# Kernel optimization log

Hardware: AMD Instinct MI355X
Metric: run time of the kernel (lower is better)

Reference implementation:

```python
import jax, jax.numpy as jnp
import numpy as np

EMBED = 256
HEADS = 8
LEVELS = 4
POINTS = 4
HD = EMBED // HEADS  # 32
SHAPES = [(100, 100), (50, 50), (25, 25), (13, 13)]  # (H, W) per level
NV = sum(h * w for h, w in SHAPES)  # 13294
BS = 2


def _lin_params(k, fan_in, fan_out):
    s = 1.0 / np.sqrt(fan_in)
    kw, kb = jax.random.split(k)
    W = jax.random.uniform(kw, (fan_in, fan_out), jnp.float32, -s, s)
    b = jax.random.uniform(kb, (fan_out,), jnp.float32, -s, s)
    return W, b


def setup_inputs():
    key = jax.random.key(0)
    ks = jax.random.split(key, 10)
    inp = {
        "query": jax.random.normal(ks[0], (BS, NV, EMBED), jnp.float32),
        "key": jax.random.normal(ks[1], (BS, NV, EMBED), jnp.float32),
        "value": jax.random.normal(ks[2], (BS, NV, EMBED), jnp.float32),
        "query_pos": jax.random.normal(ks[3], (BS, NV, EMBED), jnp.float32),
        "reference_points": jax.random.uniform(ks[4], (BS, NV, LEVELS, 2), jnp.float32),
        "spatial_shapes": jnp.array(SHAPES, jnp.int32),
        "level_start_index": jnp.array(np.cumsum([0] + [h * w for h, w in SHAPES[:-1]]), jnp.int32),
        "key_padding_mask": jnp.zeros((BS, NV), bool),
    }
    inp["W_value"], inp["b_value"] = _lin_params(ks[5], EMBED, EMBED)
    inp["W_off"], inp["b_off"] = _lin_params(ks[6], EMBED, HEADS * LEVELS * POINTS * 2)
    inp["W_attn"], inp["b_attn"] = _lin_params(ks[7], EMBED, HEADS * LEVELS * POINTS)
    inp["W_out"], inp["b_out"] = _lin_params(ks[8], EMBED, EMBED)
    inp["W_ffn"], inp["b_ffn"] = _lin_params(ks[9], EMBED, EMBED)
    return inp


def _bilinear(v, x, y, H, W):
    # v: (bs, heads, H*W, hd); x, y: (bs, heads, n) pixel coords (align_corners=False)
    # zero padding outside the feature map (matches torch grid_sample padding_mode='zeros')
    x0 = jnp.floor(x)
    y0 = jnp.floor(y)
    lx = x - x0
    ly = y - y0
    x0 = x0.astype(jnp.int32)
    y0 = y0.astype(jnp.int32)

    def g(xi, yi):
        valid = ((xi >= 0) & (xi < W) & (yi >= 0) & (yi < H)).astype(v.dtype)
        idx = jnp.clip(yi, 0, H - 1) * W + jnp.clip(xi, 0, W - 1)
        return jnp.take_along_axis(v, idx[..., None], axis=2) * valid[..., None]

    return (g(x0, y0) * ((1 - lx) * (1 - ly))[..., None]
            + g(x0 + 1, y0) * (lx * (1 - ly))[..., None]
            + g(x0, y0 + 1) * ((1 - lx) * ly)[..., None]
            + g(x0 + 1, y0 + 1) * (lx * ly)[..., None])


def _forward(query, key, value, query_pos, reference_points, shapes, starts,
             key_padding_mask, W_value, b_value, W_off, b_off, W_attn, b_attn,
             W_out, b_out, W_ffn, b_ffn):
    bs, nq, _ = query.shape
    identity = query  # residual taken BEFORE adding positional encoding (mmcv semantics)
    q = query + query_pos
    v = value @ W_value + b_value
    v = jnp.where(key_padding_mask[..., None], 0.0, v).reshape(bs, -1, HEADS, HD)
    off = (q @ W_off + b_off).reshape(bs, nq, HEADS, LEVELS, POINTS, 2)
    aw = jax.nn.softmax((q @ W_attn + b_attn).reshape(bs, nq, HEADS, LEVELS * POINTS), axis=-1)
    aw = aw.reshape(bs, nq, HEADS, LEVELS, POINTS)
    # offset normalizer is (W, H) per level
    wh = jnp.array([[w, h] for h, w in shapes], jnp.float32)
    loc = reference_points[:, :, None, :, None, :] + off / wh[None, None, None, :, None, :]
    out = jnp.zeros((bs, HEADS, nq, HD), q.dtype)
    for l, (H, W) in enumerate(shapes):
        s = starts[l]
        vl = v[:, s:s + H * W].transpose(0, 2, 1, 3)  # (bs, heads, H*W, hd)
        x = (loc[:, :, :, l, :, 0] * W - 0.5).transpose(0, 2, 1, 3).reshape(bs, HEADS, nq * POINTS)
        y = (loc[:, :, :, l, :, 1] * H - 0.5).transpose(0, 2, 1, 3).reshape(bs, HEADS, nq * POINTS)
        smp = _bilinear(vl, x, y, H, W).reshape(bs, HEADS, nq, POINTS, HD)
        wl = aw[:, :, :, l].transpose(0, 2, 1, 3)  # (bs, heads, nq, P)
        out = out + jnp.sum(smp * wl[..., None], axis=3)
    out = out.transpose(0, 2, 1, 3).reshape(bs, nq, EMBED)
    out = out @ W_out + b_out + identity
    return out @ W_ffn + b_ffn


def reference(query, key, value, query_pos, reference_points, spatial_shapes,
              level_start_index, key_padding_mask, W_value, b_value, W_off, b_off,
              W_attn, b_attn, W_out, b_out, W_ffn, b_ffn):
    # spatial shapes / level starts are structural metadata -> treat as static ints
    shapes = [tuple(int(x) for x in r) for r in np.asarray(spatial_shapes)]
    starts = [int(x) for x in np.asarray(level_start_index)]
    return _forward(query, key, value, query_pos, reference_points, shapes, starts,
                    key_padding_mask, W_value, b_value, W_off, b_off, W_attn, b_attn,
                    W_out, b_out, W_ffn, b_ffn)
```

## Files before the change

### kernel.cpp

```cpp
#include <hip/hip_runtime.h>
#include <hip/hip_bf16.h>
#include <math.h>

#define NQ 13294
#define NV 13294
#define M_ROWS (2*NQ)
#define MP 26624

typedef __attribute__((ext_vector_type(8))) short bf16x8;
typedef __attribute__((ext_vector_type(4))) float f32x4;
typedef __attribute__((ext_vector_type(2))) float f32x2;

__device__ __forceinline__ float4 ld4(const float* p){ return *(const float4*)p; }
__device__ __forceinline__ float bfu_lo(unsigned int u){ return __uint_as_float(u << 16); }
__device__ __forceinline__ float bfu_hi(unsigned int u){ return __uint_as_float(u & 0xffff0000u); }
__device__ __forceinline__ unsigned short f2bf(float f){
  unsigned int u = __float_as_uint(f);
  u += 0x7fffu + ((u >> 16) & 1u);
  return (unsigned short)(u >> 16);
}
__device__ __forceinline__ unsigned int pk2(float a, float b){
  return (unsigned int)f2bf(a) | ((unsigned int)f2bf(b) << 16);
}
__device__ __forceinline__ void gl_lds16(const unsigned short* g, unsigned short* l) {
  __builtin_amdgcn_global_load_lds(
      (const __attribute__((address_space(1))) unsigned int*)g,
      (__attribute__((address_space(3))) unsigned int*)l, 16, 0, 0);
}

__global__ __launch_bounds__(256) void prep_all(
    const float* __restrict__ value, const float* __restrict__ query,
    const float* __restrict__ qpos,
    unsigned short* __restrict__ val_bf, unsigned short* __restrict__ q_bf,
    const float* __restrict__ wv, const float* __restrict__ wo,
    const float* __restrict__ wa, const float* __restrict__ wu,
    const float* __restrict__ wf, unsigned short* __restrict__ wt)
{
  const int total = MP * 64;
  for (int i = blockIdx.x * 256 + threadIdx.x; i < total; i += gridDim.x * 256) {
    const int e = i * 4;
    ushort4 a = make_ushort4(0,0,0,0), b = make_ushort4(0,0,0,0);
    if (e < M_ROWS * 256) {
      float4 v4 = ld4(value + e);
      a = make_ushort4(f2bf(v4.x), f2bf(v4.y), f2bf(v4.z), f2bf(v4.w));
      float4 q4 = ld4(query + e);
      float4 p4 = ld4(qpos + e);
      b = make_ushort4(f2bf(q4.x+p4.x), f2bf(q4.y+p4.y), f2bf(q4.z+p4.z), f2bf(q4.w+p4.w));
    }
    *(ushort4*)(val_bf + e) = a;
    *(ushort4*)(q_bf   + e) = b;
  }
  for (int t = blockIdx.x * 256 + threadIdx.x; t < 294912; t += gridDim.x * 256) {
    const float* src; int Nn; int base;
    if      (t < 65536)  { src = wv; Nn = 256; base = 0; }
    else if (t < 131072) { src = wo; Nn = 256; base = 65536; }
    else if (t < 163840) { src = wa; Nn = 128; base = 131072; }
    else if (t < 229376) { src = wu; Nn = 256; base = 163840; }
    else                 { src = wf; Nn = 256; base = 229376; }
    const int local = t - base;
    const int n = local >> 8, k = local & 255;
    wt[t] = f2bf(src[k * Nn + n]);
  }
}

template<int NCOL, int OUT_MODE, bool ADD_RES>
__global__ __launch_bounds__(256) void gemm_gl(
    const unsigned short* __restrict__ A, const unsigned short* __restrict__ Bt,
    const float* __restrict__ biasA, const float* __restrict__ biasB,
    const float* __restrict__ RES, void* __restrict__ Cv, int N)
{
  __shared__ unsigned short lds[32768];

  const int nwg = 416 * NCOL;
  const int lin = blockIdx.x;
  const int swz = (lin & 7) * (nwg >> 3) + (lin >> 3);
  const int brow = (swz / NCOL) * 64;
  const int bcol = (swz % NCOL) * 64;

  const int tid  = threadIdx.x;
  const int wid  = tid >> 6, lane = tid & 63;
  const int wr   = wid >> 1, wc = wid & 1;
  const int fr   = lane & 15, fg = lane >> 4;

  {
    const int r0   = lane >> 3;
    const int slot = lane & 7;
    #pragma unroll
    for (int t = 0; t < 4; ++t) {
      #pragma unroll
      for (int c = 0; c < 2; ++c) {
        const int row = (wid * 2 + c) * 8 + r0;
        const int gsl = slot ^ (row & 7);
        gl_lds16(A  + (size_t)(brow + row) * 256 + t * 64 + (gsl << 3),
                 &lds[t * 4096 + (wid * 2 + c) * 512]);
        gl_lds16(Bt + (size_t)(bcol + row) * 256 + t * 64 + (gsl << 3),
                 &lds[16384 + t * 4096 + (wid * 2 + c) * 512]);
      }
    }
  }
  __syncthreads();

  f32x4 acc[2][2];
  #pragma unroll
  for (int m = 0; m < 2; ++m)
    #pragma unroll
    for (int n = 0; n < 2; ++n)
      acc[m][n] = (f32x4){0.f, 0.f, 0.f, 0.f};

  #pragma unroll
  for (int t = 0; t < 4; ++t) {
    const char* as = (const char*)&lds[t * 4096];
    const char* bs = (const char*)&lds[16384 + t * 4096];
    #pragma unroll
    for (int kk = 0; kk < 2; ++kk) {
      const int kb = kk * 64 + fg * 16;
      bf16x8 af[2], bfv[2];
      #pragma unroll
      for (int m = 0; m < 2; ++m) {
        const int r = wr * 32 + m * 16 + fr;
        af[m] = *(const bf16x8*)(as + r * 128 + (kb ^ ((r & 7) << 4)));
      }
      #pragma unroll
      for (int n = 0; n < 2; ++n) {
        const int r = wc * 32 + n * 16 + fr;
        bfv[n] = *(const bf16x8*)(bs + r * 128 + (kb ^ ((r & 7) << 4)));
      }
      #pragma unroll
      for (int m = 0; m < 2; ++m)
        #pragma unroll
        for (int n = 0; n < 2; ++n)
          acc[m][n] = __builtin_amdgcn_mfma_f32_16x16x32_bf16(af[m], bfv[n], acc[m][n], 0, 0, 0);
    }
  }

  __syncthreads();
  float* csh = (float*)lds;
  const int c0 = bcol + wc * 32 + fr;
  const int c1 = c0 + 16;
  const float bn0 = (c0 < 256) ? biasA[c0] : biasB[c0 - 256];
  const float bn1 = (c1 < 256) ? biasA[c1] : biasB[c1 - 256];
  #pragma unroll
  for (int m = 0; m < 2; ++m)
    #pragma unroll
    for (int j = 0; j < 4; ++j) {
      const int row = wr * 32 + m * 16 + fg * 4 + j;
      csh[row * 64 + wc * 32 + fr]      = acc[m][0][j] + bn0;
      csh[row * 64 + wc * 32 + 16 + fr] = acc[m][1][j] + bn1;
    }
  __syncthreads();
  #pragma unroll
  for (int i = 0; i < 4; ++i) {
    const int rl = i * 16 + (tid >> 4);
    const int gr = brow + rl;
    if (gr >= M_ROWS) continue;
    const int c4 = (tid & 15) * 4;
    float4 v = *(const float4*)&csh[rl * 64 + c4];
    if (ADD_RES) {
      float4 q = ld4(RES + (size_t)gr * 256 + bcol + c4);
      v.x += q.x; v.y += q.y; v.z += q.z; v.w += q.w;
    }
    if (OUT_MODE == 0) {
      *(float4*)&((float*)Cv)[(size_t)gr * N + bcol + c4] = v;
    } else if (OUT_MODE == 1) {
      ushort4 pk = make_ushort4(f2bf(v.x), f2bf(v.y), f2bf(v.z), f2bf(v.w));
      *(ushort4*)&((unsigned short*)Cv)[(size_t)gr * N + bcol + c4] = pk;
    } else {
      const int head = (bcol + c4) >> 5;
      const int ch   = c4 & 31;
      int r = 0;
      r = __builtin_amdgcn_cvt_pk_fp8_f32(v.x, v.y, r, 0);
      r = __builtin_amdgcn_cvt_pk_fp8_f32(v.z, v.w, r, 1);
      *(int*)&((unsigned char*)Cv)[((size_t)head * M_ROWS + gr) * 32 + ch] = r;
    }
  }
}

__global__ __launch_bounds__(256) void msda7(
    const unsigned char* __restrict__ v, const unsigned short* __restrict__ oa,
    const float* __restrict__ ref, unsigned short* __restrict__ attout)
{
  constexpr int LW[4] = {100, 50, 25, 13};
  constexpr int LS[4] = {0, 10000, 12500, 13125};

  __shared__ int2   sidx[64][17];
  __shared__ float4 swt [64][17];

  const int bid   = blockIdx.x;
  const int h     = bid & 7;
  const int chunk = bid >> 3;
  const int tid   = threadIdx.x;
  const int q     = tid >> 2;
  const int c     = tid & 3;
  const int bq    = chunk * 64 + q;
  const bool active = bq < M_ROWS;
  const int b     = (bq >= NQ) ? 1 : 0;

  if (active) {
    const int l = c;
    const int W = LW[l];
    const float fD = (float)W;
    const unsigned short* oarow = oa + (size_t)bq * 384;

    uint2 lg = *(const uint2*)(oarow + 256 + h * 16 + l * 4);
    float g0 = bfu_lo(lg.x), g1 = bfu_hi(lg.x), g2 = bfu_lo(lg.y), g3 = bfu_hi(lg.y);
    float mx = fmaxf(fmaxf(g0, g1), fmaxf(g2, g3));
    mx = fmaxf(mx, __shfl_xor(mx, 1));
    mx = fmaxf(mx, __shfl_xor(mx, 2));
    float e0 = __expf(g0-mx), e1 = __expf(g1-mx), e2 = __expf(g2-mx), e3 = __expf(g3-mx);
    float s = e0 + e1 + e2 + e3;
    s += __shfl_xor(s, 1);
    s += __shfl_xor(s, 2);
    const float inv = 1.f / s;
    const float ee[4] = {e0*inv, e1*inv, e2*inv, e3*inv};

    uint4 ov = *(const uint4*)(oarow + h * 32 + l * 8);
    const float oxy[8] = {bfu_lo(ov.x), bfu_hi(ov.x), bfu_lo(ov.y), bfu_hi(ov.y),
                          bfu_lo(ov.z), bfu_hi(ov.z), bfu_lo(ov.w), bfu_hi(ov.w)};
    const float rx = ref[(size_t)bq * 8 + l * 2];
    const float ry = ref[(size_t)bq * 8 + l * 2 + 1];
    const int rowbase = b * NV + LS[l];

    #pragma unroll
    for (int j = 0; j < 4; ++j) {
      const float x = fmaf(rx, fD, oxy[2*j])   - 0.5f;
      const float y = fmaf(ry, fD, oxy[2*j+1]) - 0.5f;
      const float x0f = floorf(x), y0f = floorf(y);
      const float lx = x - x0f, ly = y - y0f;
      const int x0 = (int)x0f, y0 = (int)y0f;
      const int y1 = y0 + 1;
      const int xbase = min(max(x0, 0), W - 2);
      const float wx0 = 1.f - lx, wx1 = lx;
      const float we0 = (x0 == xbase     ? wx0 : 0.f) + (x0 == xbase - 1 ? wx1 : 0.f);
      const float we1 = (x0 == xbase + 1 ? wx0 : 0.f) + (x0 == xbase     ? wx1 : 0.f);
      const int cy0 = min(max(y0, 0), W - 1), cy1 = min(max(y1, 0), W - 1);
      const float wy0 = (y0 >= 0 && y0 < W) ? (1.f - ly) : 0.f;
      const float wy1 = (y1 >= 0 && y1 < W) ? ly : 0.f;
      const float wt = ee[j];
      const int p = l * 4 + j;
      sidx[q][p] = make_int2((rowbase + cy0 * W + xbase) * 32,
                             (rowbase + cy1 * W + xbase) * 32);
      swt[q][p] = make_float4(wt * wy0 * we0, wt * wy0 * we1,
                              wt * wy1 * we0, wt * wy1 * we1);
    }
  }
  __syncthreads();

  if (active) {
    const unsigned char* vb = v + (size_t)h * M_ROWS * 32 + c * 16;
    const int el = c >> 1;
    f32x2 acc2[8];
    #pragma unroll
    for (int k = 0; k < 8; ++k) acc2[k] = (f32x2){0.f, 0.f};
    #pragma unroll
    for (int p = 0; p < 16; ++p) {
      const int2   ix = sidx[q][p];
      const float4 w4 = swt[q][p];
      uint4 r0 = *(const uint4*)(vb + ix.x);
      uint4 r1 = *(const uint4*)(vb + ix.y);
      const float wa = el ? w4.y : w4.x;
      const float wb = el ? w4.w : w4.z;
      const f32x2 wav = (f32x2){wa, wa};
      const f32x2 wbv = (f32x2){wb, wb};
      acc2[0] = wav * __builtin_amdgcn_cvt_pk_f32_fp8(r0.x, 0) + acc2[0];
      acc2[1] = wav * __builtin_amdgcn_cvt_pk_f32_fp8(r0.x, 1) + acc2[1];
      acc2[2] = wav * __builtin_amdgcn_cvt_pk_f32_fp8(r0.y, 0) + acc2[2];
      acc2[3] = wav * __builtin_amdgcn_cvt_pk_f32_fp8(r0.y, 1) + acc2[3];
      acc2[4] = wav * __builtin_amdgcn_cvt_pk_f32_fp8(r0.z, 0) + acc2[4];
      acc2[5] = wav * __builtin_amdgcn_cvt_pk_f32_fp8(r0.z, 1) + acc2[5];
      acc2[6] = wav * __builtin_amdgcn_cvt_pk_f32_fp8(r0.w, 0) + acc2[6];
      acc2[7] = wav * __builtin_amdgcn_cvt_pk_f32_fp8(r0.w, 1) + acc2[7];
      acc2[0] = wbv * __builtin_amdgcn_cvt_pk_f32_fp8(r1.x, 0) + acc2[0];
      acc2[1] = wbv * __builtin_amdgcn_cvt_pk_f32_fp8(r1.x, 1) + acc2[1];
      acc2[2] = wbv * __builtin_amdgcn_cvt_pk_f32_fp8(r1.y, 0) + acc2[2];
      acc2[3] = wbv * __builtin_amdgcn_cvt_pk_f32_fp8(r1.y, 1) + acc2[3];
      acc2[4] = wbv * __builtin_amdgcn_cvt_pk_f32_fp8(r1.z, 0) + acc2[4];
      acc2[5] = wbv * __builtin_amdgcn_cvt_pk_f32_fp8(r1.z, 1) + acc2[5];
      acc2[6] = wbv * __builtin_amdgcn_cvt_pk_f32_fp8(r1.w, 0) + acc2[6];
      acc2[7] = wbv * __builtin_amdgcn_cvt_pk_f32_fp8(r1.w, 1) + acc2[7];
    }
    #pragma unroll
    for (int k = 0; k < 8; ++k) {
      acc2[k][0] += __shfl_xor(acc2[k][0], 2);
      acc2[k][1] += __shfl_xor(acc2[k][1], 2);
    }
    if (c < 2) {
      uint4 pkA, pkB;
      pkA.x = pk2(acc2[0][0], acc2[0][1]);
      pkA.y = pk2(acc2[1][0], acc2[1][1]);
      pkA.z = pk2(acc2[2][0], acc2[2][1]);
      pkA.w = pk2(acc2[3][0], acc2[3][1]);
      pkB.x = pk2(acc2[4][0], acc2[4][1]);
      pkB.y = pk2(acc2[5][0], acc2[5][1]);
      pkB.z = pk2(acc2[6][0], acc2[6][1]);
      pkB.w = pk2(acc2[7][0], acc2[7][1]);
      unsigned short* dst = attout + (size_t)bq * 256 + h * 32 + c * 16;
      *(uint4*)dst = pkA;
      *(uint4*)(dst + 8) = pkB;
    }
  }
}

extern "C" void kernel_launch(void* const* d_in, const int* in_sizes, int n_in,
                              void* d_out, int out_size, void* d_ws, size_t ws_size,
                              hipStream_t stream) {
  const float* query  = (const float*)d_in[0];
  const float* value  = (const float*)d_in[2];
  const float* qpos   = (const float*)d_in[3];
  const float* refpts = (const float*)d_in[4];
  const float* W_value = (const float*)d_in[8];
  const float* b_value = (const float*)d_in[9];
  const float* W_off   = (const float*)d_in[10];
  const float* b_off   = (const float*)d_in[11];
  const float* W_attn  = (const float*)d_in[12];
  const float* b_attn  = (const float*)d_in[13];
  const float* W_out   = (const float*)d_in[14];
  const float* b_out   = (const float*)d_in[15];
  const float* W_ffn   = (const float*)d_in[16];
  const float* b_ffn   = (const float*)d_in[17];
  float* out = (float*)d_out;

  unsigned short* oa    = (unsigned short*)d_ws;
  unsigned char*  vbuf8 = (unsigned char*)(oa + (size_t)MP * 384);
  unsigned short* AB1   = (unsigned short*)(vbuf8 + (size_t)8 * M_ROWS * 32);
  unsigned short* AB2   = AB1 + (size_t)MP * 256;
  unsigned short* wts   = AB2 + (size_t)MP * 256;
  unsigned short* wv_t  = wts;
  unsigned short* woa_t = wts + 65536;
  unsigned short* wu_t  = wts + 163840;
  unsigned short* wf_t  = wts + 229376;

  const dim3 blk(256);

  prep_all<<<dim3(2048), blk, 0, stream>>>(value, query, qpos, AB1, AB2,
      W_value, W_off, W_attn, W_out, W_ffn, wts);

  gemm_gl<4,2,false><<<dim3(1664), blk, 0, stream>>>(
      AB1, wv_t, b_value, b_value, nullptr, vbuf8, 256);
  gemm_gl<6,1,false><<<dim3(2496), blk, 0, stream>>>(
      AB2, woa_t, b_off, b_attn, nullptr, oa, 384);
  msda7<<<dim3(8 * 416), blk, 0, stream>>>(vbuf8, oa, refpts, AB1);
  gemm_gl<4,1,true><<<dim3(1664), blk, 0, stream>>>(
      AB1, wu_t, b_out, b_out, query, AB2, 256);
  gemm_gl<4,0,false><<<dim3(1664), blk, 0, stream>>>(
      AB2, wf_t, b_ffn, b_ffn, nullptr, (void*)out, 256);
}
```

Before: 112.7 us.

## Fold output and FFN projections into one GEMM and merge value/offset GEMMs

Precomputes W_out·W_ffn and the combined bias inside the prep kernel, so the post-attention path becomes a single K=512 GEMM: attn_out·(W_out W_ffn) + query·W_ffn + bias. This removes one full GEMM launch and the bf16 intermediate round trip. The value-projection and offset/attention GEMMs are also merged into one launch. In exchange, prep must write an extra bf16 copy of the query and run 256 extra blocks that each do a 256-long serial dot product per thread. The fused weight is rounded to bf16 and the residual now goes through bf16, which changes numerics slightly.

```diff
diff --git a/kernel.cpp b/kernel.cpp
--- a/kernel.cpp
+++ b/kernel.cpp
@@ -32,50 +32,80 @@
     const float* __restrict__ value, const float* __restrict__ query,
     const float* __restrict__ qpos,
     unsigned short* __restrict__ val_bf, unsigned short* __restrict__ q_bf,
+    unsigned short* __restrict__ q2_bf,
     const float* __restrict__ wv, const float* __restrict__ wo,
     const float* __restrict__ wa, const float* __restrict__ wu,
-    const float* __restrict__ wf, unsigned short* __restrict__ wt)
+    const float* __restrict__ wf, unsigned short* __restrict__ wt,
+    unsigned short* __restrict__ wof_t, float* __restrict__ bias_c,
+    const float* __restrict__ b_out, const float* __restrict__ b_ffn)
 {
+  if (blockIdx.x >= 2048) {
+    const int n = blockIdx.x - 2048;
+    const int k = threadIdx.x;
+    float acc = 0.f;
+    #pragma unroll 4
+    for (int j = 0; j < 256; ++j)
+      acc = fmaf(wu[k * 256 + j], wf[j * 256 + n], acc);
+    wof_t[n * 256 + k] = f2bf(acc);
+    __shared__ float red[256];
+    red[k] = b_out[k] * wf[k * 256 + n];
+    __syncthreads();
+    #pragma unroll
+    for (int s = 128; s > 0; s >>= 1) {
+      if (k < s) red[k] += red[k + s];
+      __syncthreads();
+    }
+    if (k == 0) bias_c[n] = red[0] + b_ffn[n];
+    return;
+  }
+
   const int total = MP * 64;
-  for (int i = blockIdx.x * 256 + threadIdx.x; i < total; i += gridDim.x * 256) {
+  for (int i = blockIdx.x * 256 + threadIdx.x; i < total; i += 2048 * 256) {
     const int e = i * 4;
-    ushort4 a = make_ushort4(0,0,0,0), b = make_ushort4(0,0,0,0);
+    ushort4 a = make_ushort4(0,0,0,0), b = make_ushort4(0,0,0,0), c = make_ushort4(0,0,0,0);
     if (e < M_ROWS * 256) {
       float4 v4 = ld4(value + e);
       a = make_ushort4(f2bf(v4.x), f2bf(v4.y), f2bf(v4.z), f2bf(v4.w));
       float4 q4 = ld4(query + e);
       float4 p4 = ld4(qpos + e);
       b = make_ushort4(f2bf(q4.x+p4.x), f2bf(q4.y+p4.y), f2bf(q4.z+p4.z), f2bf(q4.w+p4.w));
+      c = make_ushort4(f2bf(q4.x), f2bf(q4.y), f2bf(q4.z), f2bf(q4.w));
     }
     *(ushort4*)(val_bf + e) = a;
     *(ushort4*)(q_bf   + e) = b;
-  }
-  for (int t = blockIdx.x * 256 + threadIdx.x; t < 294912; t += gridDim.x * 256) {
+    *(ushort4*)(q2_bf  + e) = c;
+  }
+  for (int t = blockIdx.x * 256 + threadIdx.x; t < 229376; t += 2048 * 256) {
     const float* src; int Nn; int base;
     if      (t < 65536)  { src = wv; Nn = 256; base = 0; }
     else if (t < 131072) { src = wo; Nn = 256; base = 65536; }
     else if (t < 163840) { src = wa; Nn = 128; base = 131072; }
-    else if (t < 229376) { src = wu; Nn = 256; base = 163840; }
-    else                 { src = wf; Nn = 256; base = 229376; }
+    else                 { src = wf; Nn = 256; base = 163840; }
     const int local = t - base;
     const int n = local >> 8, k = local & 255;
     wt[t] = f2bf(src[k * Nn + n]);
   }
 }
 
-template<int NCOL, int OUT_MODE, bool ADD_RES>
-__global__ __launch_bounds__(256) void gemm_gl(
-    const unsigned short* __restrict__ A, const unsigned short* __restrict__ Bt,
-    const float* __restrict__ biasA, const float* __restrict__ biasB,
-    const float* __restrict__ RES, void* __restrict__ Cv, int N)
+__global__ __launch_bounds__(256) void gemm_voa2(
+    const unsigned short* __restrict__ val_bf, const unsigned short* __restrict__ q_bf,
+    const unsigned short* __restrict__ wv_t, const unsigned short* __restrict__ woa_t,
+    const float* __restrict__ b_value, const float* __restrict__ b_off,
+    const float* __restrict__ b_attn,
+    unsigned char* __restrict__ vbuf8, unsigned short* __restrict__ oa)
 {
   __shared__ unsigned short lds[32768];
 
-  const int nwg = 416 * NCOL;
-  const int lin = blockIdx.x;
-  const int swz = (lin & 7) * (nwg >> 3) + (lin >> 3);
-  const int brow = (swz / NCOL) * 64;
-  const int bcol = (swz % NCOL) * 64;
+  const bool is_v = blockIdx.x < 1664;
+  const int  ncol = is_v ? 4 : 6;
+  const int  lin  = is_v ? blockIdx.x : blockIdx.x - 1664;
+  const int  nwg  = is_v ? 1664 : 2496;
+  const unsigned short* A  = is_v ? val_bf : q_bf;
+  const unsigned short* Bt = is_v ? wv_t : woa_t;
+
+  const int swz  = (lin & 7) * (nwg >> 3) + (lin >> 3);
+  const int brow = (swz / ncol) * 64;
+  const int bcol = (swz % ncol) * 64;
 
   const int tid  = threadIdx.x;
   const int wid  = tid >> 6, lane = tid & 63;
@@ -137,8 +167,12 @@
   float* csh = (float*)lds;
   const int c0 = bcol + wc * 32 + fr;
   const int c1 = c0 + 16;
-  const float bn0 = (c0 < 256) ? biasA[c0] : biasB[c0 - 256];
-  const float bn1 = (c1 < 256) ? biasA[c1] : biasB[c1 - 256];
+  float bn0, bn1;
+  if (is_v) { bn0 = b_value[c0]; bn1 = b_value[c1]; }
+  else {
+    bn0 = (c0 < 256) ? b_off[c0] : b_attn[c0 - 256];
+    bn1 = (c1 < 256) ? b_off[c1] : b_attn[c1 - 256];
+  }
   #pragma unroll
   for (int m = 0; m < 2; ++m)
     #pragma unroll
@@ -155,23 +189,120 @@
     if (gr >= M_ROWS) continue;
     const int c4 = (tid & 15) * 4;
     float4 v = *(const float4*)&csh[rl * 64 + c4];
-    if (ADD_RES) {
-      float4 q = ld4(RES + (size_t)gr * 256 + bcol + c4);
-      v.x += q.x; v.y += q.y; v.z += q.z; v.w += q.w;
-    }
-    if (OUT_MODE == 0) {
-      *(float4*)&((float*)Cv)[(size_t)gr * N + bcol + c4] = v;
-    } else if (OUT_MODE == 1) {
-      ushort4 pk = make_ushort4(f2bf(v.x), f2bf(v.y), f2bf(v.z), f2bf(v.w));
-      *(ushort4*)&((unsigned short*)Cv)[(size_t)gr * N + bcol + c4] = pk;
-    } else {
+    if (is_v) {
       const int head = (bcol + c4) >> 5;
       const int ch   = c4 & 31;
       int r = 0;
       r = __builtin_amdgcn_cvt_pk_fp8_f32(v.x, v.y, r, 0);
       r = __builtin_amdgcn_cvt_pk_fp8_f32(v.z, v.w, r, 1);
-      *(int*)&((unsigned char*)Cv)[((size_t)head * M_ROWS + gr) * 32 + ch] = r;
-    }
+      *(int*)&vbuf8[((size_t)head * M_ROWS + gr) * 32 + ch] = r;
+    } else {
+      ushort4 pk = make_ushort4(f2bf(v.x), f2bf(v.y), f2bf(v.z), f2bf(v.w));
+      *(ushort4*)&oa[(size_t)gr * 384 + bcol + c4] = pk;
+    }
+  }
+}
+
+__global__ __launch_bounds__(256) void gemm_final(
+    const unsigned short* __restrict__ A1, const unsigned short* __restrict__ B1,
+    const unsigned short* __restrict__ A2, const unsigned short* __restrict__ B2,
+    const float* __restrict__ bias_c, float* __restrict__ C)
+{
+  __shared__ unsigned short lds[32768];
+
+  const int nwg = 1664;
+  const int lin = blockIdx.x;
+  const int swz = (lin & 7) * (nwg >> 3) + (lin >> 3);
+  const int brow = (swz >> 2) * 64;
+  const int bcol = (swz & 3) * 64;
+
+  const int tid  = threadIdx.x;
+  const int wid  = tid >> 6, lane = tid & 63;
+  const int wr   = wid >> 1, wc = wid & 1;
+  const int fr   = lane & 15, fg = lane >> 4;
+
+  auto stage = [&](const unsigned short* A, const unsigned short* Bt) {
+    const int r0   = lane >> 3;
+    const int slot = lane & 7;
+    #pragma unroll
+    for (int t = 0; t < 4; ++t) {
+      #pragma unroll
+      for (int c = 0; c < 2; ++c) {
+        const int row = (wid * 2 + c) * 8 + r0;
+        const int gsl = slot ^ (row & 7);
+        gl_lds16(A  + (size_t)(brow + row) * 256 + t * 64 + (gsl << 3),
+                 &lds[t * 4096 + (wid * 2 + c) * 512]);
+        gl_lds16(Bt + (size_t)(bcol + row) * 256 + t * 64 + (gsl << 3),
+                 &lds[16384 + t * 4096 + (wid * 2 + c) * 512]);
+      }
+    }
+  };
+
+  f32x4 acc[2][2];
+  #pragma unroll
+  for (int m = 0; m < 2; ++m)
+    #pragma unroll
+    for (int n = 0; n < 2; ++n)
+      acc[m][n] = (f32x4){0.f, 0.f, 0.f, 0.f};
+
+  auto compute = [&]() {
+    #pragma unroll
+    for (int t = 0; t < 4; ++t) {
+      const char* as = (const char*)&lds[t * 4096];
+      const char* bs = (const char*)&lds[16384 + t * 4096];
+      #pragma unroll
+      for (int kk = 0; kk < 2; ++kk) {
+        const int kb = kk * 64 + fg * 16;
+        bf16x8 af[2], bfv[2];
+        #pragma unroll
+        for (int m = 0; m < 2; ++m) {
+          const int r = wr * 32 + m * 16 + fr;
+          af[m] = *(const bf16x8*)(as + r * 128 + (kb ^ ((r & 7) << 4)));
+        }
+        #pragma unroll
+        for (int n = 0; n < 2; ++n) {
+          const int r = wc * 32 + n * 16 + fr;
+          bfv[n] = *(const bf16x8*)(bs + r * 128 + (kb ^ ((r & 7) << 4)));
+        }
+        #pragma unroll
+        for (int m = 0; m < 2; ++m)
+          #pragma unroll
+          for (int n = 0; n < 2; ++n)
+            acc[m][n] = __builtin_amdgcn_mfma_f32_16x16x32_bf16(af[m], bfv[n], acc[m][n], 0, 0, 0);
+      }
+    }
+  };
+
+  stage(A1, B1);
+  __syncthreads();
+  compute();
+  __syncthreads();
+  stage(A2, B2);
+  __syncthreads();
+  compute();
+
+  __syncthreads();
+  float* csh = (float*)lds;
+  const int c0 = bcol + wc * 32 + fr;
+  const int c1 = c0 + 16;
+  const float bn0 = bias_c[c0];
+  const float bn1 = bias_c[c1];
+  #pragma unroll
+  for (int m = 0; m < 2; ++m)
+    #pragma unroll
+    for (int j = 0; j < 4; ++j) {
+      const int row = wr * 32 + m * 16 + fg * 4 + j;
+      csh[row * 64 + wc * 32 + fr]      = acc[m][0][j] + bn0;
+      csh[row * 64 + wc * 32 + 16 + fr] = acc[m][1][j] + bn1;
+    }
+  __syncthreads();
+  #pragma unroll
+  for (int i = 0; i < 4; ++i) {
+    const int rl = i * 16 + (tid >> 4);
+    const int gr = brow + rl;
+    if (gr >= M_ROWS) continue;
+    const int c4 = (tid & 15) * 4;
+    *(float4*)&C[(size_t)gr * 256 + bcol + c4] = *(const float4*)&csh[rl * 64 + c4];
   }
 }
 
@@ -322,25 +453,24 @@
   unsigned short* oa    = (unsigned short*)d_ws;
   unsigned char*  vbuf8 = (unsigned char*)(oa + (size_t)MP * 384);
   unsigned short* AB1   = (unsigned short*)(vbuf8 + (size_t)8 * M_ROWS * 32);
-  unsigned short* AB2   = AB1 + (size_t)MP * 256;
-  unsigned short* wts   = AB2 + (size_t)MP * 256;
+  unsigned short* QB    = AB1 + (size_t)MP * 256;
+  unsigned short* Q2B   = QB + (size_t)MP * 256;
+  unsigned short* wts   = Q2B + (size_t)MP * 256;
   unsigned short* wv_t  = wts;
   unsigned short* woa_t = wts + 65536;
-  unsigned short* wu_t  = wts + 163840;
-  unsigned short* wf_t  = wts + 229376;
+  unsigned short* wf_t  = wts + 163840;
+  unsigned short* wof_t = wts + 229376;
+  float*          bias_c = (float*)(wof_t + 65536);
 
   const dim3 blk(256);
 
-  prep_all<<<dim3(2048), blk, 0, stream>>>(value, query, qpos, AB1, AB2,
-      W_value, W_off, W_attn, W_out, W_ffn, wts);
-
-  gemm_gl<4,2,false><<<dim3(1664), blk, 0, stream>>>(
-      AB1, wv_t, b_value, b_value, nullptr, vbuf8, 256);
-  gemm_gl<6,1,false><<<dim3(2496), blk, 0, stream>>>(
-      AB2, woa_t, b_off, b_attn, nullptr, oa, 384);
+  prep_all<<<dim3(2304), blk, 0, stream>>>(value, query, qpos, AB1, QB, Q2B,
+      W_value, W_off, W_attn, W_out, W_ffn, wts, wof_t, bias_c, b_out, b_ffn);
+
+  gemm_voa2<<<dim3(1664 + 2496), blk, 0, stream>>>(
+      AB1, QB, wv_t, woa_t, b_value, b_off, b_attn, vbuf8, oa);
+
   msda7<<<dim3(8 * 416), blk, 0, stream>>>(vbuf8, oa, refpts, AB1);
-  gemm_gl<4,1,true><<<dim3(1664), blk, 0, stream>>>(
-      AB1, wu_t, b_out, b_out, query, AB2, 256);
-  gemm_gl<4,0,false><<<dim3(1664), blk, 0, stream>>>(
-      AB2, wf_t, b_ffn, b_ffn, nullptr, (void*)out, 256);
-}
+
+  gemm_final<<<dim3(1664), blk, 0, stream>>>(AB1, wof_t, Q2B, wf_t, bias_c, out);
+}
```

New measurement: 120.2 us. +6.6%, slower.
